# Performance work log

Hardware: AMD Instinct MI355X
Metric: run time of the kernel (lower is better)

## Reference

```python
import jax, jax.numpy as jnp
import numpy as np

B, N, M = 8, 4096, 4096


def setup_inputs() -> dict:
    key = jax.random.key(0)
    k1, k2 = jax.random.split(key)
    tar = jax.random.normal(k1, (B, N, 3), dtype=jnp.float32)
    src = jax.random.normal(k2, (B, M, 3), dtype=jnp.float32)
    return {"tar": tar, "src": src}


def reference(tar, src):
    # diff: [b, n, m, 3]; dist: [b, n, m] Euclidean norm
    diff = tar[:, :, None, :] - src[:, None, :, :]
    dist = jnp.sqrt(jnp.sum(diff * diff, axis=-1))
    # complete: for each target point, min over source points, mean over n -> [b]
    complete = jnp.mean(jnp.min(dist, axis=2), axis=1)
    # accuracy: for each source point, min over target points, mean over m -> [b]
    accuracy = jnp.mean(jnp.min(dist, axis=1), axis=1)
    # reduction='mean' over batch axis
    complete = jnp.mean(complete, axis=-1)
    accuracy = jnp.mean(accuracy, axis=-1)
    chamfer = 0.5 * (complete + accuracy)
    return (accuracy, complete, chamfer)
```

## Files before the change

### kernel.cpp

```cpp
#include <hip/hip_runtime.h>
#include <math.h>

#define B_ 8
#define BIGF 3.4e38f

template <int QPT, int CHUNK>
__global__ __launch_bounds__(256, 4) void minsq_kernel(
    const float* __restrict__ tar, const float* __restrict__ src,
    unsigned int* __restrict__ minarr, int N, int M)
{
    const int z   = blockIdx.z;
    const int dir = (z >= B_) ? 1 : 0;
    const int b   = dir ? (z - B_) : z;
    const float* __restrict__ qry = dir ? src : tar;
    const float* __restrict__ pts = dir ? tar : src;
    const int K = dir ? M : N;
    const int L = dir ? N : M;
    unsigned int* __restrict__ out =
        minarr + (dir ? (size_t)B_ * N : (size_t)0) + (size_t)b * K;

    const int base = blockIdx.y * CHUNK;
    if (base >= L) return;
    const int cnt = min(CHUNK, L - base);

    __shared__ float4 sp[CHUNK];
    const float* __restrict__ p3 = pts + ((size_t)b * L + base) * 3;
    const int t = threadIdx.x;
    for (int i = t; i < cnt; i += 256) {
        float x = p3[3 * i], y = p3[3 * i + 1], zc = p3[3 * i + 2];
        sp[i] = make_float4(x, y, zc, fmaf(x, x, fmaf(y, y, zc * zc)));
    }
    __syncthreads();

    const float* __restrict__ q3 = qry + (size_t)b * K * 3;
    const int qbase = blockIdx.x * (256 * QPT);
    float qx2[QPT], qy2[QPT], qz2[QPT], qw[QPT], mn[QPT];
#pragma unroll
    for (int k = 0; k < QPT; ++k) {
        int qi = qbase + k * 256 + t;
        if (qi < K) {
            float x = q3[3 * qi], y = q3[3 * qi + 1], zc = q3[3 * qi + 2];
            qx2[k] = -2.f * x; qy2[k] = -2.f * y; qz2[k] = -2.f * zc;
            qw[k] = fmaf(x, x, fmaf(y, y, zc * zc));
        } else {
            qx2[k] = 0.f; qy2[k] = 0.f; qz2[k] = 0.f; qw[k] = 0.f;
        }
        mn[k] = BIGF;
    }

    if (cnt == CHUNK) {
        float4 c0 = sp[0], c1 = sp[1];
#pragma unroll 2
        for (int j = 0; j + 2 < CHUNK; j += 2) {
            float4 n0 = sp[j + 2];
            float4 n1 = sp[j + 3];
#pragma unroll
            for (int k = 0; k < QPT; ++k) {
                float d0 = fmaf(qx2[k], c0.x, fmaf(qy2[k], c0.y,
                           fmaf(qz2[k], c0.z, c0.w)));
                float d1 = fmaf(qx2[k], c1.x, fmaf(qy2[k], c1.y,
                           fmaf(qz2[k], c1.z, c1.w)));
                mn[k] = fminf(mn[k], fminf(d0, d1));
            }
            c0 = n0; c1 = n1;
        }
#pragma unroll
        for (int k = 0; k < QPT; ++k) {
            float d0 = fmaf(qx2[k], c0.x, fmaf(qy2[k], c0.y,
                       fmaf(qz2[k], c0.z, c0.w)));
            float d1 = fmaf(qx2[k], c1.x, fmaf(qy2[k], c1.y,
                       fmaf(qz2[k], c1.z, c1.w)));
            mn[k] = fminf(mn[k], fminf(d0, d1));
        }
    } else {
        int j = 0;
        for (; j + 1 < cnt; j += 2) {
            float4 p0 = sp[j];
            float4 p1 = sp[j + 1];
#pragma unroll
            for (int k = 0; k < QPT; ++k) {
                float d0 = fmaf(qx2[k], p0.x, fmaf(qy2[k], p0.y,
                           fmaf(qz2[k], p0.z, p0.w)));
                float d1 = fmaf(qx2[k], p1.x, fmaf(qy2[k], p1.y,
                           fmaf(qz2[k], p1.z, p1.w)));
                mn[k] = fminf(mn[k], fminf(d0, d1));
            }
        }
        if (j < cnt) {
            float4 p0 = sp[j];
#pragma unroll
            for (int k = 0; k < QPT; ++k) {
                float d0 = fmaf(qx2[k], p0.x, fmaf(qy2[k], p0.y,
                           fmaf(qz2[k], p0.z, p0.w)));
                mn[k] = fminf(mn[k], d0);
            }
        }
    }

#pragma unroll
    for (int k = 0; k < QPT; ++k) {
        int qi = qbase + k * 256 + t;
        if (qi < K) {
            float d2 = fmaxf(mn[k] + qw[k], 0.f);
            atomicMin(&out[qi], __float_as_uint(d2));
        }
    }
}

__global__ __launch_bounds__(256) void reduce_kernel(
    const unsigned int* __restrict__ minarr, float* __restrict__ outp,
    int N, int M)
{
    const int nt = B_ * N, ns = B_ * M;
    const int gid = blockIdx.x * 256 + threadIdx.x;
    const int stride = gridDim.x * 256;
    float s_t = 0.f, s_s = 0.f;
    for (int i = gid; i < nt; i += stride)
        s_t += sqrtf(__uint_as_float(minarr[i]));
    for (int i = gid; i < ns; i += stride)
        s_s += sqrtf(__uint_as_float(minarr[nt + i]));
#pragma unroll
    for (int off = 32; off > 0; off >>= 1) {
        s_t += __shfl_down(s_t, off);
        s_s += __shfl_down(s_s, off);
    }
    __shared__ float rt[4], rs[4];
    const int wid = threadIdx.x >> 6, lid = threadIdx.x & 63;
    if (lid == 0) { rt[wid] = s_t; rs[wid] = s_s; }
    __syncthreads();
    if (threadIdx.x == 0) {
        float ct = (rt[0] + rt[1] + rt[2] + rt[3]) / (float)nt;
        float ac = (rs[0] + rs[1] + rs[2] + rs[3]) / (float)ns;
        atomicAdd(&outp[0], ac);
        atomicAdd(&outp[1], ct);
        atomicAdd(&outp[2], 0.5f * (ac + ct));
    }
}

extern "C" void kernel_launch(void* const* d_in, const int* in_sizes, int n_in,
                              void* d_out, int out_size, void* d_ws, size_t ws_size,
                              hipStream_t stream) {
    const float* tar = (const float*)d_in[0];
    const float* src = (const float*)d_in[1];
    const int N = in_sizes[0] / (B_ * 3);
    const int M = in_sizes[1] / (B_ * 3);

    unsigned int* minarr = (unsigned int*)d_ws;
    float* outp = (float*)d_out;

    hipMemsetAsync(minarr, 0xFF, (size_t)B_ * (N + M) * sizeof(unsigned int),
                   stream);
    hipMemsetAsync(outp, 0, 3 * sizeof(float), stream);

    constexpr int QPT = 8, CHUNK = 128;
    const int KL = (N > M) ? N : M;
    const int gx = (KL + 256 * QPT - 1) / (256 * QPT);
    const int gy = (KL + CHUNK - 1) / CHUNK;
    dim3 grid(gx, gy, 2 * B_);
    minsq_kernel<QPT, CHUNK><<<grid, dim3(256), 0, stream>>>(
        tar, src, minarr, N, M);

    reduce_kernel<<<dim3(32), dim3(256), 0, stream>>>(minarr, outp, N, M);
}
```

Baseline: 84.76 us.

## Replace atomicMin with per-chunk partial minima and drop memsets

Each block now writes its per-query minimum into a separate slice indexed by its source chunk, replacing the global atomicMin. The reduce kernel takes the min across all 32 slices before the sqrt and sum. The two memsets are removed, and the output is zeroed inside the first kernel instead. The inner loop also loses its manual software prefetch in favour of a plain unroll-4 loop. The cost is a 32x larger workspace (about 8 MB) that the reduce must stream, and zeroing the output from the first kernel depends on kernel ordering.

```diff
diff --git a/kernel.cpp b/kernel.cpp
--- a/kernel.cpp
+++ b/kernel.cpp
@@ -7,8 +7,12 @@
 template <int QPT, int CHUNK>
 __global__ __launch_bounds__(256, 4) void minsq_kernel(
     const float* __restrict__ tar, const float* __restrict__ src,
-    unsigned int* __restrict__ minarr, int N, int M)
+    float* __restrict__ partial, float* __restrict__ outp, int N, int M)
 {
+    if (blockIdx.x == 0 && blockIdx.y == 0 && blockIdx.z == 0 &&
+        threadIdx.x < 3)
+        outp[threadIdx.x] = 0.f;
+
     const int z   = blockIdx.z;
     const int dir = (z >= B_) ? 1 : 0;
     const int b   = dir ? (z - B_) : z;
@@ -16,12 +20,15 @@
     const float* __restrict__ pts = dir ? tar : src;
     const int K = dir ? M : N;
     const int L = dir ? N : M;
-    unsigned int* __restrict__ out =
-        minarr + (dir ? (size_t)B_ * N : (size_t)0) + (size_t)b * K;
 
     const int base = blockIdx.y * CHUNK;
     if (base >= L) return;
     const int cnt = min(CHUNK, L - base);
+
+    const size_t SL = (size_t)B_ * (N + M);
+    float* __restrict__ out = partial + (size_t)blockIdx.y * SL +
+                              (dir ? (size_t)B_ * N : (size_t)0) +
+                              (size_t)b * K;
 
     __shared__ float4 sp[CHUNK];
     const float* __restrict__ p3 = pts + ((size_t)b * L + base) * 3;
@@ -49,28 +56,18 @@
     }
 
     if (cnt == CHUNK) {
-        float4 c0 = sp[0], c1 = sp[1];
-#pragma unroll 2
-        for (int j = 0; j + 2 < CHUNK; j += 2) {
-            float4 n0 = sp[j + 2];
-            float4 n1 = sp[j + 3];
+#pragma unroll 4
+        for (int j = 0; j < CHUNK; j += 2) {
+            float4 p0 = sp[j];
+            float4 p1 = sp[j + 1];
 #pragma unroll
             for (int k = 0; k < QPT; ++k) {
-                float d0 = fmaf(qx2[k], c0.x, fmaf(qy2[k], c0.y,
-                           fmaf(qz2[k], c0.z, c0.w)));
-                float d1 = fmaf(qx2[k], c1.x, fmaf(qy2[k], c1.y,
-                           fmaf(qz2[k], c1.z, c1.w)));
+                float d0 = fmaf(qx2[k], p0.x, fmaf(qy2[k], p0.y,
+                           fmaf(qz2[k], p0.z, p0.w)));
+                float d1 = fmaf(qx2[k], p1.x, fmaf(qy2[k], p1.y,
+                           fmaf(qz2[k], p1.z, p1.w)));
                 mn[k] = fminf(mn[k], fminf(d0, d1));
             }
-            c0 = n0; c1 = n1;
-        }
-#pragma unroll
-        for (int k = 0; k < QPT; ++k) {
-            float d0 = fmaf(qx2[k], c0.x, fmaf(qy2[k], c0.y,
-                       fmaf(qz2[k], c0.z, c0.w)));
-            float d1 = fmaf(qx2[k], c1.x, fmaf(qy2[k], c1.y,
-                       fmaf(qz2[k], c1.z, c1.w)));
-            mn[k] = fminf(mn[k], fminf(d0, d1));
         }
     } else {
         int j = 0;
@@ -100,25 +97,34 @@
 #pragma unroll
     for (int k = 0; k < QPT; ++k) {
         int qi = qbase + k * 256 + t;
-        if (qi < K) {
-            float d2 = fmaxf(mn[k] + qw[k], 0.f);
-            atomicMin(&out[qi], __float_as_uint(d2));
-        }
+        if (qi < K) out[qi] = fmaxf(mn[k] + qw[k], 0.f);
     }
 }
 
+template <int CHUNK>
 __global__ __launch_bounds__(256) void reduce_kernel(
-    const unsigned int* __restrict__ minarr, float* __restrict__ outp,
+    const float* __restrict__ partial, float* __restrict__ outp,
     int N, int M)
 {
     const int nt = B_ * N, ns = B_ * M;
+    const size_t SL = (size_t)nt + ns;
+    const int slT = (M + CHUNK - 1) / CHUNK;
+    const int slS = (N + CHUNK - 1) / CHUNK;
     const int gid = blockIdx.x * 256 + threadIdx.x;
     const int stride = gridDim.x * 256;
     float s_t = 0.f, s_s = 0.f;
-    for (int i = gid; i < nt; i += stride)
-        s_t += sqrtf(__uint_as_float(minarr[i]));
-    for (int i = gid; i < ns; i += stride)
-        s_s += sqrtf(__uint_as_float(minarr[nt + i]));
+    for (int i = gid; i < nt; i += stride) {
+        float v = BIGF;
+        for (int s = 0; s < slT; ++s)
+            v = fminf(v, partial[(size_t)s * SL + i]);
+        s_t += sqrtf(v);
+    }
+    for (int i = gid; i < ns; i += stride) {
+        float v = BIGF;
+        for (int s = 0; s < slS; ++s)
+            v = fminf(v, partial[(size_t)s * SL + nt + i]);
+        s_s += sqrtf(v);
+    }
 #pragma unroll
     for (int off = 32; off > 0; off >>= 1) {
         s_t += __shfl_down(s_t, off);
@@ -145,12 +151,8 @@
     const int N = in_sizes[0] / (B_ * 3);
     const int M = in_sizes[1] / (B_ * 3);
 
-    unsigned int* minarr = (unsigned int*)d_ws;
+    float* partial = (float*)d_ws;
     float* outp = (float*)d_out;
-
-    hipMemsetAsync(minarr, 0xFF, (size_t)B_ * (N + M) * sizeof(unsigned int),
-                   stream);
-    hipMemsetAsync(outp, 0, 3 * sizeof(float), stream);
 
     constexpr int QPT = 8, CHUNK = 128;
     const int KL = (N > M) ? N : M;
@@ -158,7 +160,8 @@
     const int gy = (KL + CHUNK - 1) / CHUNK;
     dim3 grid(gx, gy, 2 * B_);
     minsq_kernel<QPT, CHUNK><<<grid, dim3(256), 0, stream>>>(
-        tar, src, minarr, N, M);
+        tar, src, partial, outp, N, M);
 
-    reduce_kernel<<<dim3(32), dim3(256), 0, stream>>>(minarr, outp, N, M);
+    reduce_kernel<CHUNK><<<dim3(64), dim3(256), 0, stream>>>(
+        partial, outp, N, M);
 }
```

Measured after the change: 101.1 us. 1.19x slower.
